# Kernel optimization log

Measured on AMD Instinct MI355X. Metric: run time of the kernel, lower is better.

## Reference

```python
import jax, jax.numpy as jnp
import numpy as np

N_NODES = 10000
N_EDGES = 320000
F = 128
N_RBF = 20


def setup_inputs() -> dict:
    key = jax.random.key(0)
    ks = jax.random.split(key, 12)
    inp = {
        "idx_i": jax.random.randint(ks[0], (N_EDGES,), 0, N_NODES),
        "idx_j": jax.random.randint(ks[1], (N_EDGES,), 0, N_NODES),
        "rel_dir": jax.random.normal(ks[2], (N_EDGES, 3), dtype=jnp.float32),
        "rel_dist_cut": jax.random.uniform(ks[3], (N_EDGES,), dtype=jnp.float32),
        "rbf_features": jax.random.normal(ks[4], (N_EDGES, N_RBF), dtype=jnp.float32),
        "scalar_features": jax.random.normal(ks[5], (N_NODES, F), dtype=jnp.float32),
        "vector_features": jax.random.normal(ks[6], (N_NODES, F, 3), dtype=jnp.float32),
        # learned params: scalar_network = Linear(F,F) -> SiLU -> Linear(F,3F); rbf_network = Linear(N_RBF,3F)
        "W1": jax.random.normal(ks[7], (F, F), dtype=jnp.float32) / np.sqrt(F),
        "b1": jnp.zeros((F,), dtype=jnp.float32),
        "W2": jax.random.normal(ks[8], (F, 3 * F), dtype=jnp.float32) / np.sqrt(F),
        "b2": jnp.zeros((3 * F,), dtype=jnp.float32),
        "Wr": jax.random.normal(ks[9], (N_RBF, 3 * F), dtype=jnp.float32) / np.sqrt(N_RBF),
        "br": jnp.zeros((3 * F,), dtype=jnp.float32),
    }
    return inp


def reference(idx_i, idx_j, rel_dir, rel_dist_cut, rbf_features,
              scalar_features, vector_features, W1, b1, W2, b2, Wr, br):
    num_nodes, num_features = scalar_features.shape
    # per-node MLP: [N, 3F]
    phi = jax.nn.silu(scalar_features @ W1 + b1) @ W2 + b2
    # distance gate: [E, 3F]
    Wg = (rbf_features @ Wr + br) * rel_dist_cut[:, None]
    # gather neighbor phi and gate
    phi_W = phi[idx_j] * Wg                       # [E, 3F]
    phi_W_vv = phi_W[:, :num_features]            # [E, F]
    phi_W_ss = phi_W[:, num_features:2 * num_features]
    phi_W_vs = phi_W[:, 2 * num_features:]
    # per-receiver edge counts (bincount)
    counts = jax.ops.segment_sum(jnp.ones((idx_i.shape[0],), phi_W.dtype),
                                 idx_i, num_segments=num_nodes)  # [N]
    scalar_residuals = jax.ops.segment_sum(phi_W_ss, idx_i, num_segments=num_nodes)
    scalar_residuals = scalar_residuals / counts[:, None]
    # per-edge vector message: [E, F, 3]
    v_edge = (vector_features[idx_j] * phi_W_vv[:, :, None]
              + phi_W_vs[:, :, None] * rel_dir[:, None, :])
    vector_residuals = jax.ops.segment_sum(v_edge, idx_i, num_segments=num_nodes)
    vector_residuals = vector_residuals / counts[:, None, None]
    return (scalar_features + scalar_residuals,
            vector_features + vector_residuals)
```

## Files before the change

kernel.cpp:

```cpp
#include <hip/hip_runtime.h>
#include <hip/hip_bf16.h>

#define NN 10000
#define NE 320000
#define FDIM 128
#define NRBF 20
#define PHI_DIM 384
#define NKEY NN
#define SCAN_BLOCKS 40

typedef unsigned int uint;
typedef unsigned short ushort;

#if __has_builtin(__builtin_amdgcn_fdot2_f32_bf16)
#define USE_DOT2 1
typedef __bf16 bf16x2 __attribute__((ext_vector_type(2)));
#else
#define USE_DOT2 0
#endif

__device__ __forceinline__ ushort f2bf(float x) {
  __hip_bfloat16 b = __float2bfloat16(x);
  return *(ushort*)&b;
}


__global__ void phi_kernel(const float* __restrict__ S, const float* __restrict__ W1,
                           const float* __restrict__ b1, const float* __restrict__ W2,
                           const float* __restrict__ b2, const float* __restrict__ vf,
                           const int* __restrict__ idx_i, int* __restrict__ counts,
                           char* __restrict__ tab) {
  __shared__ float s_s[8][FDIM];
  __shared__ float h_s[8][FDIM];
  const int t = threadIdx.x;
  const int n0 = blockIdx.x * 8;
  {
    const int e0 = (blockIdx.x * 128 + t) * 2;
    atomicAdd(&counts[idx_i[e0]], 1);
    atomicAdd(&counts[idx_i[e0 + 1]], 1);
  }
#pragma unroll
  for (int n = 0; n < 8; n++) s_s[n][t] = S[(n0 + n) * FDIM + t];
  __syncthreads();
  float acc[8];
#pragma unroll
  for (int n = 0; n < 8; n++) acc[n] = 0.f;
  for (int k = 0; k < FDIM; k++) {
    float w = W1[k * FDIM + t];
#pragma unroll
    for (int n = 0; n < 8; n++) acc[n] += s_s[n][k] * w;
  }
  float bb = b1[t];
#pragma unroll
  for (int n = 0; n < 8; n++) {
    float x = acc[n] + bb;
    h_s[n][t] = x / (1.0f + expf(-x));
  }
  __syncthreads();
  float a0[8], a1[8], a2[8];
#pragma unroll
  for (int n = 0; n < 8; n++) { a0[n] = 0.f; a1[n] = 0.f; a2[n] = 0.f; }
  for (int k = 0; k < FDIM; k++) {
    float w0 = W2[k * PHI_DIM + t];
    float w1 = W2[k * PHI_DIM + t + 128];
    float w2 = W2[k * PHI_DIM + t + 256];
#pragma unroll
    for (int n = 0; n < 8; n++) {
      float hv = h_s[n][k];
      a0[n] += hv * w0;
      a1[n] += hv * w1;
      a2[n] += hv * w2;
    }
  }
  float c0 = b2[t], c1 = b2[t + 128], c2 = b2[t + 256];
#pragma unroll
  for (int n = 0; n < 8; n++) {
    const int node = n0 + n;
    const float p0 = a0[n] + c0;
    const float p1 = a1[n] + c1;
    const float p2 = a2[n] + c2;
    const float* src = vf + (size_t)node * (FDIM * 3) + t * 3;
    const uint wx = f2bf(src[0] * p0);
    const uint wy = f2bf(src[1] * p0);
    const uint wz = f2bf(src[2] * p0);
    char* pb = tab + (size_t)node * 1280;
    ((uint*)pb)[t] = (wy << 16) | wx;
    ((uint*)(pb + 512))[t] = ((uint)f2bf(p1) << 16) | wz;
    ((ushort*)(pb + 1024))[t] = f2bf(p2);
  }
}

__global__ void scan1_kernel(const int* __restrict__ counts, int* __restrict__ offsets,
                             int* __restrict__ blocksums) {
  __shared__ int s[256];
  const int t = threadIdx.x;
  const int idx = blockIdx.x * 256 + t;
  const int c = counts[idx];
  s[t] = c;
  __syncthreads();
  for (int off = 1; off < 256; off <<= 1) {
    int v = (t >= off) ? s[t - off] : 0;
    __syncthreads();
    s[t] += v;
    __syncthreads();
  }
  if (idx < NKEY) offsets[idx] = s[t] - c;
  if (t == 255) blocksums[blockIdx.x] = s[255];
}

__global__ void scan2_kernel(int* __restrict__ blocksums, int* __restrict__ offsets) {
  __shared__ int s[64];
  const int t = threadIdx.x;
  int v0 = (t < SCAN_BLOCKS) ? blocksums[t] : 0;
  s[t] = v0;
  __syncthreads();
  for (int off = 1; off < 64; off <<= 1) {
    int v = (t >= off) ? s[t - off] : 0;
    __syncthreads();
    s[t] += v;
    __syncthreads();
  }
  if (t < SCAN_BLOCKS) blocksums[t] = s[t] - v0;
  if (t == SCAN_BLOCKS - 1) offsets[NKEY] = s[t];
}

__global__ void scan3_kernel(int* __restrict__ offsets, const int* __restrict__ blocksums) {
  const int idx = blockIdx.x * 256 + threadIdx.x;
  if (idx < NKEY) offsets[idx] += blocksums[blockIdx.x];
}

__global__ void stage_kernel(const int* __restrict__ idx_i, const int* __restrict__ idx_j,
                             const float* __restrict__ cut, const float* __restrict__ dir,
                             const float* __restrict__ rbf, const int* __restrict__ offsets,
                             int* __restrict__ counts, uint* __restrict__ edata,
                             int* __restrict__ jlist) {
  int e = blockIdx.x * blockDim.x + threadIdx.x;
  if (e >= NE) return;
  int i = idx_i[e];
  int pos = atomicSub(&counts[i], 1) - 1;
  const int slot = offsets[i] + pos;
  const int j = idx_j[e];
  jlist[slot] = j;
  uint* d = edata + (size_t)slot * 16;
  const float c = cut[e];
  d[0] = (uint)j;
  d[1] = __float_as_uint(c);
  d[2] = __float_as_uint(dir[e * 3 + 0]);
  d[3] = __float_as_uint(dir[e * 3 + 1]);
  d[4] = __float_as_uint(dir[e * 3 + 2]);
  d[5] = 0u;
  const float* rb = rbf + (size_t)e * NRBF;
#pragma unroll
  for (int r = 0; r < 10; r++) {
    uint lo = (uint)f2bf(rb[2 * r] * c);
    uint hi = (uint)f2bf(rb[2 * r + 1] * c);
    d[6 + r] = (hi << 16) | lo;
  }
}

__global__ __launch_bounds__(128, 5) void node_kernel(
    const uint* __restrict__ edata, const int* __restrict__ jlist,
    const float* __restrict__ Wr, const float* __restrict__ br,
    const char* __restrict__ tab, const float* __restrict__ sf,
    const float* __restrict__ vf, const int* __restrict__ offsets,
    float* __restrict__ out) {
  const int f = threadIdx.x;
#if USE_DOT2
  bf16x2 wrA[10], wrB[10], wrC[10];
#pragma unroll
  for (int r = 0; r < 10; r++) {
    uint a = ((uint)f2bf(Wr[(2 * r + 1) * PHI_DIM + f]) << 16) | f2bf(Wr[(2 * r) * PHI_DIM + f]);
    uint b = ((uint)f2bf(Wr[(2 * r + 1) * PHI_DIM + f + 128]) << 16) |
             f2bf(Wr[(2 * r) * PHI_DIM + f + 128]);
    uint c = ((uint)f2bf(Wr[(2 * r + 1) * PHI_DIM + f + 256]) << 16) |
             f2bf(Wr[(2 * r) * PHI_DIM + f + 256]);
    wrA[r] = __builtin_bit_cast(bf16x2, a);
    wrB[r] = __builtin_bit_cast(bf16x2, b);
    wrC[r] = __builtin_bit_cast(bf16x2, c);
  }
#else
  float wrA[NRBF], wrB[NRBF], wrC[NRBF];
#pragma unroll
  for (int r = 0; r < NRBF; r++) {
    wrA[r] = Wr[r * PHI_DIM + f];
    wrB[r] = Wr[r * PHI_DIM + f + 128];
    wrC[r] = Wr[r * PHI_DIM + f + 256];
  }
#endif
  const int n = blockIdx.x;
  const int beg = offsets[n], end = offsets[n + 1];
  const float br0 = br[f], br1 = br[f + 128], br2 = br[f + 256];
  float ss = 0.f, ax = 0.f, ay = 0.f, az = 0.f;
  const int f4 = f * 4;

  auto process = [&](const uint4* rec, uint d0, uint d1, uint zu) {
    uint4 q0 = rec[0];
    uint4 q1 = rec[1];
    uint4 q2 = rec[2];
    uint4 q3 = rec[3];
    const float c = __uint_as_float(q0.y);
    const float dx = __uint_as_float(q0.z);
    const float dy = __uint_as_float(q0.w);
    const float dz = __uint_as_float(q1.x);
    uint rbp[10] = {q1.z, q1.w, q2.x, q2.y, q2.z, q2.w, q3.x, q3.y, q3.z, q3.w};
    float g0 = 0.f, g1 = 0.f, g2 = 0.f;
#if USE_DOT2
#pragma unroll
    for (int r = 0; r < 10; r++) {
      bf16x2 rp = __builtin_bit_cast(bf16x2, rbp[r]);
      g0 = __builtin_amdgcn_fdot2_f32_bf16(rp, wrA[r], g0, false);
      g1 = __builtin_amdgcn_fdot2_f32_bf16(rp, wrB[r], g1, false);
      g2 = __builtin_amdgcn_fdot2_f32_bf16(rp, wrC[r], g2, false);
    }
#else
#pragma unroll
    for (int r = 0; r < 10; r++) {
      float rlo = __uint_as_float(rbp[r] << 16);
      float rhi = __uint_as_float(rbp[r] & 0xffff0000u);
      g0 += rlo * wrA[2 * r] + rhi * wrA[2 * r + 1];
      g1 += rlo * wrB[2 * r] + rhi * wrB[2 * r + 1];
      g2 += rlo * wrC[2 * r] + rhi * wrC[2 * r + 1];
    }
#endif
    g0 += br0 * c;
    g1 += br1 * c;
    g2 += br2 * c;
    const float wx = __uint_as_float(d0 << 16);
    const float wy = __uint_as_float(d0 & 0xffff0000u);
    const float wz = __uint_as_float(d1 << 16);
    const float p1 = __uint_as_float(d1 & 0xffff0000u);
    const float p2 = __uint_as_float(zu << 16);
    const float vs = p2 * g2;
    ss += p1 * g1;
    ax += wx * g0 + vs * dx;
    ay += wy * g0 + vs * dy;
    az += wz * g0 + vs * dz;
  };

  int p = beg;
  for (; p + 2 <= end; p += 2) {
    const int j0 = jlist[p];
    const int j1 = jlist[p + 1];
    const char* B0 = tab + (size_t)j0 * 1280;
    const char* B1 = tab + (size_t)j1 * 1280;
    const uint d00 = *(const uint*)(B0 + f4);
    const uint d01 = *(const uint*)(B0 + 512 + f4);
    const uint z0 = *(const ushort*)(B0 + 1024 + f * 2);
    const uint d10 = *(const uint*)(B1 + f4);
    const uint d11 = *(const uint*)(B1 + 512 + f4);
    const uint z1 = *(const ushort*)(B1 + 1024 + f * 2);
    const uint4* r0 = (const uint4*)(edata + (size_t)p * 16);
    const uint4* r1 = (const uint4*)(edata + (size_t)(p + 1) * 16);
    process(r0, d00, d01, z0);
    process(r1, d10, d11, z1);
  }
  if (p < end) {
    const int j0 = jlist[p];
    const char* B0 = tab + (size_t)j0 * 1280;
    const uint d00 = *(const uint*)(B0 + f4);
    const uint d01 = *(const uint*)(B0 + 512 + f4);
    const uint z0 = *(const ushort*)(B0 + 1024 + f * 2);
    process((const uint4*)(edata + (size_t)p * 16), d00, d01, z0);
  }

  const float inv = 1.0f / (float)(end - beg);
  out[(size_t)n * FDIM + f] = sf[(size_t)n * FDIM + f] + ss * inv;
  float* ov = out + (size_t)NN * FDIM + (size_t)n * (FDIM * 3) + f * 3;
  const float* iv = vf + (size_t)n * (FDIM * 3) + f * 3;
  ov[0] = iv[0] + ax * inv;
  ov[1] = iv[1] + ay * inv;
  ov[2] = iv[2] + az * inv;
}

extern "C" void kernel_launch(void* const* d_in, const int* in_sizes, int n_in,
                              void* d_out, int out_size, void* d_ws, size_t ws_size,
                              hipStream_t stream) {
  const int* idx_i = (const int*)d_in[0];
  const int* idx_j = (const int*)d_in[1];
  const float* rel_dir = (const float*)d_in[2];
  const float* cut = (const float*)d_in[3];
  const float* rbf = (const float*)d_in[4];
  const float* sf = (const float*)d_in[5];
  const float* vf = (const float*)d_in[6];
  const float* W1 = (const float*)d_in[7];
  const float* b1 = (const float*)d_in[8];
  const float* W2 = (const float*)d_in[9];
  const float* b2 = (const float*)d_in[10];
  const float* Wr = (const float*)d_in[11];
  const float* br = (const float*)d_in[12];
  float* out = (float*)d_out;

  char* w = (char*)d_ws;
  int* counts = (int*)w;
  int* offsets = (int*)(w + 40960);
  int* blocksums = (int*)(w + 81920);
  uint* edata = (uint*)(w + 90112);
  char* tab = w + 20570112;
  int* jlist = (int*)(w + 33370112);

  hipMemsetAsync(w, 0, 40960, stream);
  hipLaunchKernelGGL(phi_kernel, dim3(NN / 8), dim3(128), 0, stream, sf, W1, b1, W2, b2, vf,
                     idx_i, counts, tab);
  hipLaunchKernelGGL(scan1_kernel, dim3(SCAN_BLOCKS), dim3(256), 0, stream, counts, offsets,
                     blocksums);
  hipLaunchKernelGGL(scan2_kernel, dim3(1), dim3(64), 0, stream, blocksums, offsets);
  hipLaunchKernelGGL(scan3_kernel, dim3(SCAN_BLOCKS), dim3(256), 0, stream, offsets, blocksums);
  hipLaunchKernelGGL(stage_kernel, dim3((NE + 255) / 256), dim3(256), 0, stream, idx_i, idx_j,
                     cut, rel_dir, rbf, offsets, counts, edata, jlist);
  hipLaunchKernelGGL(node_kernel, dim3(NN), dim3(128), 0, stream, edata, jlist, Wr, br, tab, sf,
                     vf, offsets, out);
}
```

Before: 168.2 us.

## Compress edge records to 48 bytes, fold bias into dot, unroll node loop

Edge records are repacked into three uint4s: direction and cutoff become bf16, and the bias is folded into the bf16 dot product as an extra term paired with the cutoff. This cuts the per-edge bytes read in the node kernel. The node loop is unrolled to four edges to expose more gather parallelism, and the phi kernel uses four nodes per block for more blocks. Reducing direction and cutoff to bf16 adds small precision loss.

```diff
diff --git a/kernel.cpp b/kernel.cpp
--- a/kernel.cpp
+++ b/kernel.cpp
@@ -23,6 +23,8 @@
   __hip_bfloat16 b = __float2bfloat16(x);
   return *(ushort*)&b;
 }
+__device__ __forceinline__ float bflo(uint u) { return __uint_as_float(u << 16); }
+__device__ __forceinline__ float bfhi(uint u) { return __uint_as_float(u & 0xffff0000u); }
 
 
 __global__ void phi_kernel(const float* __restrict__ S, const float* __restrict__ W1,
@@ -30,42 +32,38 @@
                            const float* __restrict__ b2, const float* __restrict__ vf,
                            const int* __restrict__ idx_i, int* __restrict__ counts,
                            char* __restrict__ tab) {
-  __shared__ float s_s[8][FDIM];
-  __shared__ float h_s[8][FDIM];
+  __shared__ float s_s[4][FDIM];
+  __shared__ float h_s[4][FDIM];
   const int t = threadIdx.x;
-  const int n0 = blockIdx.x * 8;
-  {
-    const int e0 = (blockIdx.x * 128 + t) * 2;
-    atomicAdd(&counts[idx_i[e0]], 1);
-    atomicAdd(&counts[idx_i[e0 + 1]], 1);
-  }
-#pragma unroll
-  for (int n = 0; n < 8; n++) s_s[n][t] = S[(n0 + n) * FDIM + t];
+  const int n0 = blockIdx.x * 4;
+  atomicAdd(&counts[idx_i[blockIdx.x * 128 + t]], 1);
+#pragma unroll
+  for (int n = 0; n < 4; n++) s_s[n][t] = S[(n0 + n) * FDIM + t];
   __syncthreads();
-  float acc[8];
-#pragma unroll
-  for (int n = 0; n < 8; n++) acc[n] = 0.f;
+  float acc[4];
+#pragma unroll
+  for (int n = 0; n < 4; n++) acc[n] = 0.f;
   for (int k = 0; k < FDIM; k++) {
     float w = W1[k * FDIM + t];
 #pragma unroll
-    for (int n = 0; n < 8; n++) acc[n] += s_s[n][k] * w;
+    for (int n = 0; n < 4; n++) acc[n] += s_s[n][k] * w;
   }
   float bb = b1[t];
 #pragma unroll
-  for (int n = 0; n < 8; n++) {
+  for (int n = 0; n < 4; n++) {
     float x = acc[n] + bb;
     h_s[n][t] = x / (1.0f + expf(-x));
   }
   __syncthreads();
-  float a0[8], a1[8], a2[8];
-#pragma unroll
-  for (int n = 0; n < 8; n++) { a0[n] = 0.f; a1[n] = 0.f; a2[n] = 0.f; }
+  float a0[4], a1[4], a2[4];
+#pragma unroll
+  for (int n = 0; n < 4; n++) { a0[n] = 0.f; a1[n] = 0.f; a2[n] = 0.f; }
   for (int k = 0; k < FDIM; k++) {
     float w0 = W2[k * PHI_DIM + t];
     float w1 = W2[k * PHI_DIM + t + 128];
     float w2 = W2[k * PHI_DIM + t + 256];
 #pragma unroll
-    for (int n = 0; n < 8; n++) {
+    for (int n = 0; n < 4; n++) {
       float hv = h_s[n][k];
       a0[n] += hv * w0;
       a1[n] += hv * w1;
@@ -74,7 +72,7 @@
   }
   float c0 = b2[t], c1 = b2[t + 128], c2 = b2[t + 256];
 #pragma unroll
-  for (int n = 0; n < 8; n++) {
+  for (int n = 0; n < 4; n++) {
     const int node = n0 + n;
     const float p0 = a0[n] + c0;
     const float p1 = a1[n] + c1;
@@ -139,23 +137,22 @@
   int i = idx_i[e];
   int pos = atomicSub(&counts[i], 1) - 1;
   const int slot = offsets[i] + pos;
-  const int j = idx_j[e];
-  jlist[slot] = j;
-  uint* d = edata + (size_t)slot * 16;
+  jlist[slot] = idx_j[e];
   const float c = cut[e];
-  d[0] = (uint)j;
-  d[1] = __float_as_uint(c);
-  d[2] = __float_as_uint(dir[e * 3 + 0]);
-  d[3] = __float_as_uint(dir[e * 3 + 1]);
-  d[4] = __float_as_uint(dir[e * 3 + 2]);
-  d[5] = 0u;
+  uint w[12];
+  w[0] = ((uint)f2bf(dir[e * 3 + 1]) << 16) | f2bf(dir[e * 3 + 0]);
   const float* rb = rbf + (size_t)e * NRBF;
 #pragma unroll
   for (int r = 0; r < 10; r++) {
     uint lo = (uint)f2bf(rb[2 * r] * c);
     uint hi = (uint)f2bf(rb[2 * r + 1] * c);
-    d[6 + r] = (hi << 16) | lo;
-  }
+    w[1 + r] = (hi << 16) | lo;
+  }
+  w[11] = ((uint)f2bf(dir[e * 3 + 2]) << 16) | f2bf(c);
+  uint4* d = (uint4*)(edata + (size_t)slot * 12);
+  d[0] = make_uint4(w[0], w[1], w[2], w[3]);
+  d[1] = make_uint4(w[4], w[5], w[6], w[7]);
+  d[2] = make_uint4(w[8], w[9], w[10], w[11]);
 }
 
 __global__ __launch_bounds__(128, 5) void node_kernel(
@@ -166,7 +163,7 @@
     float* __restrict__ out) {
   const int f = threadIdx.x;
 #if USE_DOT2
-  bf16x2 wrA[10], wrB[10], wrC[10];
+  bf16x2 wrA[11], wrB[11], wrC[11];
 #pragma unroll
   for (int r = 0; r < 10; r++) {
     uint a = ((uint)f2bf(Wr[(2 * r + 1) * PHI_DIM + f]) << 16) | f2bf(Wr[(2 * r) * PHI_DIM + f]);
@@ -178,35 +175,35 @@
     wrB[r] = __builtin_bit_cast(bf16x2, b);
     wrC[r] = __builtin_bit_cast(bf16x2, c);
   }
+  wrA[10] = __builtin_bit_cast(bf16x2, (uint)f2bf(br[f]));
+  wrB[10] = __builtin_bit_cast(bf16x2, (uint)f2bf(br[f + 128]));
+  wrC[10] = __builtin_bit_cast(bf16x2, (uint)f2bf(br[f + 256]));
 #else
-  float wrA[NRBF], wrB[NRBF], wrC[NRBF];
+  float wrA[22], wrB[22], wrC[22];
 #pragma unroll
   for (int r = 0; r < NRBF; r++) {
     wrA[r] = Wr[r * PHI_DIM + f];
     wrB[r] = Wr[r * PHI_DIM + f + 128];
     wrC[r] = Wr[r * PHI_DIM + f + 256];
   }
+  wrA[20] = br[f];      wrA[21] = 0.f;
+  wrB[20] = br[f + 128]; wrB[21] = 0.f;
+  wrC[20] = br[f + 256]; wrC[21] = 0.f;
 #endif
   const int n = blockIdx.x;
   const int beg = offsets[n], end = offsets[n + 1];
-  const float br0 = br[f], br1 = br[f + 128], br2 = br[f + 256];
   float ss = 0.f, ax = 0.f, ay = 0.f, az = 0.f;
   const int f4 = f * 4;
 
-  auto process = [&](const uint4* rec, uint d0, uint d1, uint zu) {
-    uint4 q0 = rec[0];
-    uint4 q1 = rec[1];
-    uint4 q2 = rec[2];
-    uint4 q3 = rec[3];
-    const float c = __uint_as_float(q0.y);
-    const float dx = __uint_as_float(q0.z);
-    const float dy = __uint_as_float(q0.w);
-    const float dz = __uint_as_float(q1.x);
-    uint rbp[10] = {q1.z, q1.w, q2.x, q2.y, q2.z, q2.w, q3.x, q3.y, q3.z, q3.w};
+  auto process = [&](uint4 e0, uint4 e1, uint4 e2, uint d0, uint d1, uint zu) {
+    uint rbp[11] = {e0.y, e0.z, e0.w, e1.x, e1.y, e1.z, e1.w, e2.x, e2.y, e2.z, e2.w};
+    const float dx = bflo(e0.x);
+    const float dy = bfhi(e0.x);
+    const float dz = bfhi(rbp[10]);
     float g0 = 0.f, g1 = 0.f, g2 = 0.f;
 #if USE_DOT2
 #pragma unroll
-    for (int r = 0; r < 10; r++) {
+    for (int r = 0; r < 11; r++) {
       bf16x2 rp = __builtin_bit_cast(bf16x2, rbp[r]);
       g0 = __builtin_amdgcn_fdot2_f32_bf16(rp, wrA[r], g0, false);
       g1 = __builtin_amdgcn_fdot2_f32_bf16(rp, wrB[r], g1, false);
@@ -214,53 +211,60 @@
     }
 #else
 #pragma unroll
-    for (int r = 0; r < 10; r++) {
-      float rlo = __uint_as_float(rbp[r] << 16);
-      float rhi = __uint_as_float(rbp[r] & 0xffff0000u);
+    for (int r = 0; r < 11; r++) {
+      float rlo = bflo(rbp[r]);
+      float rhi = bfhi(rbp[r]);
       g0 += rlo * wrA[2 * r] + rhi * wrA[2 * r + 1];
       g1 += rlo * wrB[2 * r] + rhi * wrB[2 * r + 1];
       g2 += rlo * wrC[2 * r] + rhi * wrC[2 * r + 1];
     }
 #endif
-    g0 += br0 * c;
-    g1 += br1 * c;
-    g2 += br2 * c;
-    const float wx = __uint_as_float(d0 << 16);
-    const float wy = __uint_as_float(d0 & 0xffff0000u);
-    const float wz = __uint_as_float(d1 << 16);
-    const float p1 = __uint_as_float(d1 & 0xffff0000u);
-    const float p2 = __uint_as_float(zu << 16);
-    const float vs = p2 * g2;
-    ss += p1 * g1;
-    ax += wx * g0 + vs * dx;
-    ay += wy * g0 + vs * dy;
-    az += wz * g0 + vs * dz;
+    const float vs = bflo(zu) * g2;
+    ss += bfhi(d1) * g1;
+    ax += bflo(d0) * g0 + vs * dx;
+    ay += bfhi(d0) * g0 + vs * dy;
+    az += bflo(d1) * g0 + vs * dz;
   };
 
   int p = beg;
-  for (; p + 2 <= end; p += 2) {
-    const int j0 = jlist[p];
-    const int j1 = jlist[p + 1];
+  for (; p + 4 <= end; p += 4) {
+    const int j0 = jlist[p], j1 = jlist[p + 1], j2 = jlist[p + 2], j3 = jlist[p + 3];
     const char* B0 = tab + (size_t)j0 * 1280;
     const char* B1 = tab + (size_t)j1 * 1280;
-    const uint d00 = *(const uint*)(B0 + f4);
-    const uint d01 = *(const uint*)(B0 + 512 + f4);
+    const char* B2 = tab + (size_t)j2 * 1280;
+    const char* B3 = tab + (size_t)j3 * 1280;
+    const uint d00 = *(const uint*)(B0 + f4), d01 = *(const uint*)(B0 + 512 + f4);
     const uint z0 = *(const ushort*)(B0 + 1024 + f * 2);
-    const uint d10 = *(const uint*)(B1 + f4);
-    const uint d11 = *(const uint*)(B1 + 512 + f4);
+    const uint d10 = *(const uint*)(B1 + f4), d11 = *(const uint*)(B1 + 512 + f4);
     const uint z1 = *(const ushort*)(B1 + 1024 + f * 2);
-    const uint4* r0 = (const uint4*)(edata + (size_t)p * 16);
-    const uint4* r1 = (const uint4*)(edata + (size_t)(p + 1) * 16);
-    process(r0, d00, d01, z0);
-    process(r1, d10, d11, z1);
-  }
-  if (p < end) {
+    const uint d20 = *(const uint*)(B2 + f4), d21 = *(const uint*)(B2 + 512 + f4);
+    const uint z2 = *(const ushort*)(B2 + 1024 + f * 2);
+    const uint d30 = *(const uint*)(B3 + f4), d31 = *(const uint*)(B3 + 512 + f4);
+    const uint z3 = *(const ushort*)(B3 + 1024 + f * 2);
+    {
+      const uint4* r0 = (const uint4*)(edata + (size_t)p * 12);
+      const uint4* r1 = (const uint4*)(edata + (size_t)(p + 1) * 12);
+      uint4 a0 = r0[0], a1 = r0[1], a2 = r0[2];
+      uint4 b0 = r1[0], b1 = r1[1], b2 = r1[2];
+      process(a0, a1, a2, d00, d01, z0);
+      process(b0, b1, b2, d10, d11, z1);
+    }
+    {
+      const uint4* r2 = (const uint4*)(edata + (size_t)(p + 2) * 12);
+      const uint4* r3 = (const uint4*)(edata + (size_t)(p + 3) * 12);
+      uint4 a0 = r2[0], a1 = r2[1], a2 = r2[2];
+      uint4 b0 = r3[0], b1 = r3[1], b2 = r3[2];
+      process(a0, a1, a2, d20, d21, z2);
+      process(b0, b1, b2, d30, d31, z3);
+    }
+  }
+  for (; p < end; p++) {
     const int j0 = jlist[p];
     const char* B0 = tab + (size_t)j0 * 1280;
-    const uint d00 = *(const uint*)(B0 + f4);
-    const uint d01 = *(const uint*)(B0 + 512 + f4);
+    const uint d00 = *(const uint*)(B0 + f4), d01 = *(const uint*)(B0 + 512 + f4);
     const uint z0 = *(const ushort*)(B0 + 1024 + f * 2);
-    process((const uint4*)(edata + (size_t)p * 16), d00, d01, z0);
+    const uint4* r0 = (const uint4*)(edata + (size_t)p * 12);
+    process(r0[0], r0[1], r0[2], d00, d01, z0);
   }
 
   const float inv = 1.0f / (float)(end - beg);
@@ -295,11 +299,11 @@
   int* offsets = (int*)(w + 40960);
   int* blocksums = (int*)(w + 81920);
   uint* edata = (uint*)(w + 90112);
-  char* tab = w + 20570112;
-  int* jlist = (int*)(w + 33370112);
+  char* tab = w + 15450112;
+  int* jlist = (int*)(w + 28250112);
 
   hipMemsetAsync(w, 0, 40960, stream);
-  hipLaunchKernelGGL(phi_kernel, dim3(NN / 8), dim3(128), 0, stream, sf, W1, b1, W2, b2, vf,
+  hipLaunchKernelGGL(phi_kernel, dim3(NN / 4), dim3(128), 0, stream, sf, W1, b1, W2, b2, vf,
                      idx_i, counts, tab);
   hipLaunchKernelGGL(scan1_kernel, dim3(SCAN_BLOCKS), dim3(256), 0, stream, counts, offsets,
                      blocksums);
```

Measured after the change: 170.4 us. About the same (+1.3%).
